# Performance work log

Measured on AMD Instinct MI355X. Metric: run time of the kernel, lower is better.

## Reference

```python
import jax, jax.numpy as jnp
import numpy as np

S, B, H, A = 64, 128, 768, 768


def setup_inputs() -> dict:
    key = jax.random.key(0)
    k1, k2, k3, k4, k5, k6, k7 = jax.random.split(key, 7)
    lim = 1.0 / np.sqrt(H)  # torch Linear default init range
    return {
        "topic_output": jax.random.normal(k1, (1, B, H), dtype=jnp.float32),
        "image_output": jax.random.normal(k2, (S, B, H), dtype=jnp.float32),
        "text_output": jax.random.normal(k3, (S, B, H), dtype=jnp.float32),
        "Wq": jax.random.uniform(k4, (H, A), minval=-lim, maxval=lim, dtype=jnp.float32),
        "bq": jax.random.uniform(k5, (A,), minval=-lim, maxval=lim, dtype=jnp.float32),
        "Wv": jax.random.uniform(k6, (S, H, A), minval=-lim, maxval=lim, dtype=jnp.float32),
        "bv": jax.random.uniform(k7, (S, A), minval=-lim, maxval=lim, dtype=jnp.float32),
    }


def reference(topic_output, image_output, text_output, Wq, bq, Wv, bv):
    # Q = topic_q(topic_output).transpose(0,1) -> [B, 1, A]; we keep it [B, A]
    topic = topic_output[0]                      # [B, H]
    Q = topic @ Wq + bq                          # [B, A]

    # Per step i: atten_input = [topic; image_i; text_i] -> [3, B, H]; V_i = v[i](atten_input)
    # Batched over all steps as grouped GEMMs with the per-step weight stack Wv [S, H, A].
    V_topic = jnp.einsum('bh,sha->sba', topic, Wv)        # [S, B, A]
    V_img = jnp.einsum('sbh,sha->sba', image_output, Wv)  # [S, B, A]
    V_txt = jnp.einsum('sbh,sha->sba', text_output, Wv)   # [S, B, A]
    V = jnp.stack([V_topic, V_img, V_txt], axis=2) + bv[:, None, None, :]  # [S, B, 3, A]

    norm = jnp.asarray(1.0 / np.sqrt(A), dtype=Q.dtype)
    scores = jnp.einsum('ba,sbka->sbk', Q, V) * norm       # [S, B, 3]
    attn = jax.nn.softmax(scores, axis=-1)
    return jnp.einsum('sbk,sbka->sba', attn, V)            # [S, B, A]
```

## Files before the change

kernel.cpp:

```cpp
#include <hip/hip_runtime.h>
#include <hip/hip_bf16.h>
#include <math.h>

#define S_ 64
#define B_ 128
#define H_ 768
#define A_ 768

typedef __bf16 bf16_t;
typedef __attribute__((ext_vector_type(8))) __bf16 bf16x8;
typedef __attribute__((ext_vector_type(4))) __bf16 bf16x4;
typedef __attribute__((ext_vector_type(2))) __bf16 bf16x2;
typedef __attribute__((ext_vector_type(4))) float f32x4;

#define TOPIC_N   98304
#define IMG_N   6291456

__device__ __forceinline__ bf16x8 pack8(float4 a, float4 b) {
    bf16x8 o;
    o[0]=(bf16_t)a.x; o[1]=(bf16_t)a.y; o[2]=(bf16_t)a.z; o[3]=(bf16_t)a.w;
    o[4]=(bf16_t)b.x; o[5]=(bf16_t)b.y; o[6]=(bf16_t)b.z; o[7]=(bf16_t)b.w;
    return o;
}

__device__ __forceinline__ void glds16b(const bf16_t* g, bf16_t* l) {
    __builtin_amdgcn_global_load_lds(
        (const __attribute__((address_space(1))) uint32_t*)g,
        (__attribute__((address_space(3))) uint32_t*)l, 16, 0, 0);
}


__global__ __launch_bounds__(256)
void convert_kernel(const float* __restrict__ topic, const float* __restrict__ image,
                    const float* __restrict__ text, bf16_t* __restrict__ out) {
    const int i = blockIdx.x * 256 + threadIdx.x;
    const int T8 = TOPIC_N / 8, I8 = IMG_N / 8;
    const size_t e = (size_t)i * 8;
    const float* src; size_t off;
    if (i < T8)           { src = topic; off = e; }
    else if (i < T8 + I8) { src = image; off = e - TOPIC_N; }
    else                  { src = text;  off = e - TOPIC_N - IMG_N; }
    const float4* p = reinterpret_cast<const float4*>(src + off);
    float4 a = p[0], b = p[1];
    *reinterpret_cast<bf16x8*>(out + e) = pack8(a, b);
}

__global__ __launch_bounds__(512, 4)
void gemm_fused(const float* __restrict__ Wv, const float* __restrict__ Wq,
                const bf16_t* __restrict__ actB,
                const float* __restrict__ bq, const float* __restrict__ bv,
                bf16_t* __restrict__ Vws, float* __restrict__ Qws)
{
    __shared__ bf16_t Al[2][128 * 64];
    __shared__ bf16_t Bl[2][192 * 64];

    const int b0 = blockIdx.x;
    const int xcd = b0 & 7, ii = b0 >> 3;
    const int bid = (xcd < 4) ? (xcd * 97 + ii) : (388 + (xcd - 4) * 96 + ii);

    const int tid = threadIdx.x;
    const bool isQ = (bid >= 768);
    int s, tm, tn;
    if (isQ) { s = S_; tm = 0; tn = bid - 768; }
    else     { s = bid / 12; const int t = bid % 12; tm = t / 4; tn = t % 4; }

    const bf16_t* Apanel;
    if (isQ || tm == 0) Apanel = actB;
    else if (tm == 1)   Apanel = actB + TOPIC_N + (size_t)s * B_ * H_;
    else                Apanel = actB + TOPIC_N + IMG_N + (size_t)s * B_ * H_;
    const float* Wbase = (isQ ? Wq : (Wv + (size_t)s * H_ * A_)) + tn * 192;

    const int wv = tid >> 6, lane = tid & 63;
    const int wr = wv >> 2, wc = wv & 3;
    const int fr = lane & 15, fg = lane >> 4;

    const int wp  = tid >> 4;
    const int wg  = tid & 15;
    const int wk0 = 2 * wp;

    f32x4 acc[4][3];
    #pragma unroll
    for (int i = 0; i < 4; ++i)
        #pragma unroll
        for (int j = 0; j < 3; ++j)
            acc[i][j] = (f32x4){0.f, 0.f, 0.f, 0.f};

    auto stageA = [&](int t1, int buf) {
        const int k0 = t1 * 64;
        #pragma unroll
        for (int q = 0; q < 2; ++q) {
            const int slot = (q * 8 + wv) * 64 + lane;
            const int row = slot >> 3, c = slot & 7;
            glds16b(Apanel + (size_t)row * H_ + k0 + ((c ^ (row & 7)) * 8),
                    &Al[buf][(q * 8 + wv) * 512]);
        }
    };

    f32x4 wreg[6];
    auto loadW = [&](int t1) {
        const float* base = Wbase + (size_t)(t1 * 64 + wk0) * A_;
        #pragma unroll
        for (int j = 0; j < 3; ++j) {
            wreg[2*j]   = *reinterpret_cast<const f32x4*>(base +        wg * 4 + 64 * j);
            wreg[2*j+1] = *reinterpret_cast<const f32x4*>(base + A_ +   wg * 4 + 64 * j);
        }
    };
    auto writeB = [&](int buf) {
        #pragma unroll
        for (int j = 0; j < 3; ++j)
            #pragma unroll
            for (int i = 0; i < 4; ++i) {
                const int n   = wg * 4 + 64 * j + i;
                const int key = (n ^ (n >> 3)) & 7;
                const int kx  = (((wk0 >> 3) ^ key) << 3) + (wk0 & 7);
                bf16x2 pr;
                pr[0] = (bf16_t)wreg[2*j][i];
                pr[1] = (bf16_t)wreg[2*j+1][i];
                *reinterpret_cast<bf16x2*>(&Bl[buf][n * 64 + kx]) = pr;
            }
    };

    loadW(0);
    stageA(0, 0);
    writeB(0);
    asm volatile("s_waitcnt vmcnt(0) lgkmcnt(0)" ::: "memory");
    __builtin_amdgcn_sched_barrier(0);
    __builtin_amdgcn_s_barrier();
    __builtin_amdgcn_sched_barrier(0);

    #pragma unroll
    for (int t = 0; t < 12; ++t) {
        const int cur = t & 1, nxt = cur ^ 1;
        if (t < 11) {
            loadW(t + 1);
            stageA(t + 1, nxt);
        }
        __builtin_amdgcn_sched_barrier(0);

        #pragma unroll
        for (int kk = 0; kk < 2; ++kk) {
            bf16x8 af[4], bf_[3];
            const int kb = kk * 4 + fg;
            #pragma unroll
            for (int mi = 0; mi < 4; ++mi) {
                const int m = wr * 64 + mi * 16 + fr;
                af[mi] = *reinterpret_cast<const bf16x8*>(
                    &Al[cur][m * 64 + ((kb ^ (m & 7)) << 3)]);
            }
            #pragma unroll
            for (int ni = 0; ni < 3; ++ni) {
                const int n   = wc * 48 + ni * 16 + fr;
                const int key = (n ^ (n >> 3)) & 7;
                bf_[ni] = *reinterpret_cast<const bf16x8*>(
                    &Bl[cur][n * 64 + ((kb ^ key) << 3)]);
            }
            #pragma unroll
            for (int mi = 0; mi < 4; ++mi)
                #pragma unroll
                for (int ni = 0; ni < 3; ++ni)
                    acc[mi][ni] = __builtin_amdgcn_mfma_f32_16x16x32_bf16(
                        af[mi], bf_[ni], acc[mi][ni], 0, 0, 0);
        }
        __builtin_amdgcn_sched_barrier(0);

        if (t < 11) {
            writeB(nxt);
            asm volatile("s_waitcnt vmcnt(0) lgkmcnt(0)" ::: "memory");
            __builtin_amdgcn_sched_barrier(0);
            __builtin_amdgcn_s_barrier();
            __builtin_amdgcn_sched_barrier(0);
        }
    }

    if (isQ) {
        #pragma unroll
        for (int ni = 0; ni < 3; ++ni) {
            const int n = tn * 192 + wc * 48 + ni * 16 + fr;
            const float bias = bq[n];
            #pragma unroll
            for (int mi = 0; mi < 4; ++mi)
                #pragma unroll
                for (int j = 0; j < 4; ++j) {
                    const int m = wr * 64 + mi * 16 + fg * 4 + j;
                    Qws[(size_t)m * A_ + n] = acc[mi][ni][j] + bias;
                }
        }
    } else {
        const float* bvrow = bv + (size_t)s * A_;
        #pragma unroll
        for (int ni = 0; ni < 3; ++ni) {
            const int n = tn * 192 + wc * 48 + ni * 16 + fr;
            const float bias = bvrow[n];
            #pragma unroll
            for (int mi = 0; mi < 4; ++mi)
                #pragma unroll
                for (int j = 0; j < 4; ++j) {
                    const int b = wr * 64 + mi * 16 + fg * 4 + j;
                    Vws[(((size_t)s * B_ + b) * 3 + tm) * A_ + n] = (bf16_t)(acc[mi][ni][j] + bias);
                }
        }
    }
}

__global__ __launch_bounds__(256)
void mm_attn_kernel(const bf16_t* __restrict__ Vws,
                    const float* __restrict__ Qws,
                    float* __restrict__ out)
{
    const int wave = threadIdx.x >> 6;
    const int lane = threadIdx.x & 63;
    const int p = blockIdx.x * 4 + wave;
    const int s = p >> 7;
    const int b = p & 127;
    const float*  qrow  = Qws + (size_t)b * A_;
    const bf16_t* vbase = Vws + ((size_t)s * B_ + b) * 3 * A_;

    float4 qv[3];
    bf16x4 vv[3][3];
    float p0 = 0.f, p1 = 0.f, p2 = 0.f;
    #pragma unroll
    for (int j = 0; j < 3; ++j) {
        const int a = lane * 4 + j * 256;
        qv[j]    = *reinterpret_cast<const float4*>(qrow + a);
        vv[0][j] = *reinterpret_cast<const bf16x4*>(vbase + 0*A_ + a);
        vv[1][j] = *reinterpret_cast<const bf16x4*>(vbase + 1*A_ + a);
        vv[2][j] = *reinterpret_cast<const bf16x4*>(vbase + 2*A_ + a);
        p0 += qv[j].x*(float)vv[0][j][0] + qv[j].y*(float)vv[0][j][1]
            + qv[j].z*(float)vv[0][j][2] + qv[j].w*(float)vv[0][j][3];
        p1 += qv[j].x*(float)vv[1][j][0] + qv[j].y*(float)vv[1][j][1]
            + qv[j].z*(float)vv[1][j][2] + qv[j].w*(float)vv[1][j][3];
        p2 += qv[j].x*(float)vv[2][j][0] + qv[j].y*(float)vv[2][j][1]
            + qv[j].z*(float)vv[2][j][2] + qv[j].w*(float)vv[2][j][3];
    }
    #pragma unroll
    for (int d = 1; d < 64; d <<= 1) {
        p0 += __shfl_xor(p0, d);
        p1 += __shfl_xor(p1, d);
        p2 += __shfl_xor(p2, d);
    }
    const float norm = 0.03608439182435161f;
    const float s0 = p0 * norm, s1 = p1 * norm, s2 = p2 * norm;
    const float mx = fmaxf(s0, fmaxf(s1, s2));
    const float e0 = expf(s0 - mx), e1 = expf(s1 - mx), e2 = expf(s2 - mx);
    const float inv = 1.f / (e0 + e1 + e2);
    const float a0 = e0 * inv, a1 = e1 * inv, a2 = e2 * inv;

    float* orow = out + ((size_t)s * B_ + b) * A_;
    #pragma unroll
    for (int j = 0; j < 3; ++j) {
        const int a = lane * 4 + j * 256;
        float4 o;
        o.x = a0*(float)vv[0][j][0] + a1*(float)vv[1][j][0] + a2*(float)vv[2][j][0];
        o.y = a0*(float)vv[0][j][1] + a1*(float)vv[1][j][1] + a2*(float)vv[2][j][1];
        o.z = a0*(float)vv[0][j][2] + a1*(float)vv[1][j][2] + a2*(float)vv[2][j][2];
        o.w = a0*(float)vv[0][j][3] + a1*(float)vv[1][j][3] + a2*(float)vv[2][j][3];
        *reinterpret_cast<float4*>(orow + a) = o;
    }
}

#define LDSPAD 40
__global__ __launch_bounds__(256, 2)
void mm_gemm_kernel(const float* __restrict__ topic,
                    const float* __restrict__ image,
                    const float* __restrict__ text,
                    const float* __restrict__ Wq,
                    const float* __restrict__ bq,
                    const float* __restrict__ Wv,
                    const float* __restrict__ bv,
                    bf16_t* __restrict__ Vws,
                    float*  __restrict__ Qws)
{
    __shared__ bf16_t Alds[128][LDSPAD];
    __shared__ bf16_t Blds[128][LDSPAD];

    const int bid = blockIdx.x;
    const int tid = threadIdx.x;
    const bool isQ = (bid >= S_ * 18);
    int s, tm, tn;
    if (isQ) { s = 0; tm = 0; tn = bid - S_ * 18; }
    else     { s = bid / 18; const int t = bid % 18; tm = t / 6; tn = t % 6; }

    const int ar  = tid >> 1;
    const int aks = (tid & 1) * 16;
    const float* arow;
    if (isQ) {
        arow = topic + (size_t)ar * H_;
    } else {
        const int am  = tm * 128 + ar;
        const int sel = am >> 7;
        const int b   = am & 127;
        if (sel == 0)      arow = topic + (size_t)b * H_;
        else if (sel == 1) arow = image + ((size_t)s * B_ + b) * H_;
        else               arow = text  + ((size_t)s * B_ + b) * H_;
    }
    const int arot = (ar >> 3) & 3;

    const int bn  = tid & 127;
    const int bks = (tid >> 7) * 16;
    const float* wbase = isQ ? Wq : (Wv + (size_t)s * H_ * A_);
    const float* bcolp = wbase + (size_t)(tn * 128 + bn);
    const int brot = (bn >> 3) & 3;

    const int wave = tid >> 6;
    const int lane = tid & 63;
    const int wr = wave >> 1;
    const int wc = wave & 1;
    const int fr = lane & 15;
    const int fg = lane >> 4;

    f32x4 acc[4][4];
    #pragma unroll
    for (int i = 0; i < 4; ++i)
        #pragma unroll
        for (int j = 0; j < 4; ++j)
            acc[i][j] = (f32x4){0.f, 0.f, 0.f, 0.f};

    for (int k0 = 0; k0 < H_; k0 += 32) {
        float4 av[4];
        const float4* ap = reinterpret_cast<const float4*>(arow + k0 + aks);
        #pragma unroll
        for (int i = 0; i < 4; ++i) av[i] = ap[i];
        float bvr[16];
        #pragma unroll
        for (int j = 0; j < 16; ++j) bvr[j] = bcolp[(size_t)(k0 + bks + j) * A_];

        __syncthreads();

        #pragma unroll
        for (int i = 0; i < 4; ++i) {
            const int j = (i + arot) & 3;
            bf16x4 c;
            c[0] = (bf16_t)av[j].x; c[1] = (bf16_t)av[j].y;
            c[2] = (bf16_t)av[j].z; c[3] = (bf16_t)av[j].w;
            *reinterpret_cast<bf16x4*>(&Alds[ar][aks + 4*j]) = c;
        }
        #pragma unroll
        for (int i = 0; i < 4; ++i) {
            const int j = (i + brot) & 3;
            bf16x4 c;
            c[0] = (bf16_t)bvr[4*j+0]; c[1] = (bf16_t)bvr[4*j+1];
            c[2] = (bf16_t)bvr[4*j+2]; c[3] = (bf16_t)bvr[4*j+3];
            *reinterpret_cast<bf16x4*>(&Blds[bn][bks + 4*j]) = c;
        }
        __syncthreads();

        bf16x8 afrag[4], bfrag[4];
        #pragma unroll
        for (int mi = 0; mi < 4; ++mi)
            afrag[mi] = *reinterpret_cast<const bf16x8*>(&Alds[wr*64 + mi*16 + fr][fg*8]);
        #pragma unroll
        for (int ni = 0; ni < 4; ++ni)
            bfrag[ni] = *reinterpret_cast<const bf16x8*>(&Blds[wc*64 + ni*16 + fr][fg*8]);
        #pragma unroll
        for (int mi = 0; mi < 4; ++mi)
            #pragma unroll
            for (int ni = 0; ni < 4; ++ni)
                acc[mi][ni] = __builtin_amdgcn_mfma_f32_16x16x32_bf16(
                    afrag[mi], bfrag[ni], acc[mi][ni], 0, 0, 0);
    }

    if (isQ) {
        #pragma unroll
        for (int ni = 0; ni < 4; ++ni) {
            const int n = tn*128 + wc*64 + ni*16 + fr;
            const float bias = bq[n];
            #pragma unroll
            for (int mi = 0; mi < 4; ++mi)
                #pragma unroll
                for (int j = 0; j < 4; ++j) {
                    const int m = wr*64 + mi*16 + fg*4 + j;
                    Qws[(size_t)m * A_ + n] = acc[mi][ni][j] + bias;
                }
        }
    } else {
        const float* bvrow = bv + (size_t)s * A_;
        #pragma unroll
        for (int ni = 0; ni < 4; ++ni) {
            const int n = tn*128 + wc*64 + ni*16 + fr;
            const float bias = bvrow[n];
            #pragma unroll
            for (int mi = 0; mi < 4; ++mi)
                #pragma unroll
                for (int j = 0; j < 4; ++j) {
                    const int b = wr*64 + mi*16 + fg*4 + j;
                    Vws[(((size_t)s * B_ + b) * 3 + tm) * A_ + n] = (bf16_t)(acc[mi][ni][j] + bias);
                }
        }
    }
}

extern "C" void kernel_launch(void* const* d_in, const int* in_sizes, int n_in,
                              void* d_out, int out_size, void* d_ws, size_t ws_size,
                              hipStream_t stream)
{
    const float* topic = (const float*)d_in[0];
    const float* image = (const float*)d_in[1];
    const float* text  = (const float*)d_in[2];
    const float* Wq    = (const float*)d_in[3];
    const float* bq    = (const float*)d_in[4];
    const float* Wv    = (const float*)d_in[5];
    const float* bv    = (const float*)d_in[6];
    float* out = (float*)d_out;

    const size_t szAct = (size_t)(TOPIC_N + 2 * IMG_N) * sizeof(bf16_t);
    const size_t szV   = (size_t)S_ * B_ * 3 * A_ * sizeof(bf16_t);
    const size_t szQ   = (size_t)B_ * A_ * sizeof(float);
    const size_t need  = szAct + szV + szQ;

    if (ws_size >= need) {
        char* w = (char*)d_ws;
        bf16_t* actB = (bf16_t*)w;  w += szAct;
        bf16_t* Vws  = (bf16_t*)w;  w += szV;
        float*  Qws  = (float*) w;

        convert_kernel<<<(TOPIC_N + 2 * IMG_N) / 8 / 256, 256, 0, stream>>>(topic, image, text, actB);
        gemm_fused<<<772, 512, 0, stream>>>(Wv, Wq, actB, bq, bv, Vws, Qws);
        mm_attn_kernel<<<S_ * B_ / 4, 256, 0, stream>>>(Vws, Qws, out);
    } else {
        bf16_t* Vws = (bf16_t*)d_ws;
        float*  Qws = (float*)((char*)d_ws + szV);
        mm_gemm_kernel<<<S_ * 18 + 6, 256, 0, stream>>>(topic, image, text, Wq, bq, Wv, bv, Vws, Qws);
        mm_attn_kernel<<<S_ * B_ / 4, 256, 0, stream>>>(Vws, Qws, out);
    }
}
```

Before: 92.92 us.

## Fuse fp32-to-bf16 activation conversion into GEMM with register-staged prefetch

Removes the separate conversion kernel and its bf16 activation workspace. The GEMM now loads fp32 activations straight into registers and converts them to bf16 while writing LDS, in the same way weights were already handled. Global loads are issued two tiles ahead, so the wait before each barrier only covers LDS traffic. This saves a kernel launch and a full write and re-read of the converted activations. In exchange each block reads twice as many bytes of fp32 activation and carries more registers for prefetch, which may limit occupancy.

After: 151.5 us. +63.0%, slower.

```diff
diff --git a/kernel.cpp b/kernel.cpp
--- a/kernel.cpp
+++ b/kernel.cpp
@@ -13,43 +13,20 @@
 typedef __attribute__((ext_vector_type(2))) __bf16 bf16x2;
 typedef __attribute__((ext_vector_type(4))) float f32x4;
 
-#define TOPIC_N   98304
-#define IMG_N   6291456
-
-__device__ __forceinline__ bf16x8 pack8(float4 a, float4 b) {
+__device__ __forceinline__ bf16x8 pack8(f32x4 a, f32x4 b) {
     bf16x8 o;
-    o[0]=(bf16_t)a.x; o[1]=(bf16_t)a.y; o[2]=(bf16_t)a.z; o[3]=(bf16_t)a.w;
-    o[4]=(bf16_t)b.x; o[5]=(bf16_t)b.y; o[6]=(bf16_t)b.z; o[7]=(bf16_t)b.w;
+    o[0]=(bf16_t)a[0]; o[1]=(bf16_t)a[1]; o[2]=(bf16_t)a[2]; o[3]=(bf16_t)a[3];
+    o[4]=(bf16_t)b[0]; o[5]=(bf16_t)b[1]; o[6]=(bf16_t)b[2]; o[7]=(bf16_t)b[3];
     return o;
 }
 
-__device__ __forceinline__ void glds16b(const bf16_t* g, bf16_t* l) {
-    __builtin_amdgcn_global_load_lds(
-        (const __attribute__((address_space(1))) uint32_t*)g,
-        (__attribute__((address_space(3))) uint32_t*)l, 16, 0, 0);
-}
-
-
-__global__ __launch_bounds__(256)
-void convert_kernel(const float* __restrict__ topic, const float* __restrict__ image,
-                    const float* __restrict__ text, bf16_t* __restrict__ out) {
-    const int i = blockIdx.x * 256 + threadIdx.x;
-    const int T8 = TOPIC_N / 8, I8 = IMG_N / 8;
-    const size_t e = (size_t)i * 8;
-    const float* src; size_t off;
-    if (i < T8)           { src = topic; off = e; }
-    else if (i < T8 + I8) { src = image; off = e - TOPIC_N; }
-    else                  { src = text;  off = e - TOPIC_N - IMG_N; }
-    const float4* p = reinterpret_cast<const float4*>(src + off);
-    float4 a = p[0], b = p[1];
-    *reinterpret_cast<bf16x8*>(out + e) = pack8(a, b);
-}
 
 __global__ __launch_bounds__(512, 4)
-void gemm_fused(const float* __restrict__ Wv, const float* __restrict__ Wq,
-                const bf16_t* __restrict__ actB,
-                const float* __restrict__ bq, const float* __restrict__ bv,
-                bf16_t* __restrict__ Vws, float* __restrict__ Qws)
+void gemm_all(const float* __restrict__ topic, const float* __restrict__ image,
+              const float* __restrict__ text,  const float* __restrict__ Wq,
+              const float* __restrict__ Wv,
+              const float* __restrict__ bq, const float* __restrict__ bv,
+              bf16_t* __restrict__ Vws, float* __restrict__ Qws)
 {
     __shared__ bf16_t Al[2][128 * 64];
     __shared__ bf16_t Bl[2][192 * 64];
@@ -64,19 +41,22 @@
     if (isQ) { s = S_; tm = 0; tn = bid - 768; }
     else     { s = bid / 12; const int t = bid % 12; tm = t / 4; tn = t % 4; }
 
-    const bf16_t* Apanel;
-    if (isQ || tm == 0) Apanel = actB;
-    else if (tm == 1)   Apanel = actB + TOPIC_N + (size_t)s * B_ * H_;
-    else                Apanel = actB + TOPIC_N + IMG_N + (size_t)s * B_ * H_;
+    const float* Apanel;
+    if (isQ || tm == 0) Apanel = topic;
+    else if (tm == 1)   Apanel = image + (size_t)s * B_ * H_;
+    else                Apanel = text  + (size_t)s * B_ * H_;
     const float* Wbase = (isQ ? Wq : (Wv + (size_t)s * H_ * A_)) + tn * 192;
 
     const int wv = tid >> 6, lane = tid & 63;
     const int wr = wv >> 2, wc = wv & 3;
     const int fr = lane & 15, fg = lane >> 4;
 
-    const int wp  = tid >> 4;
+    const int ar  = tid >> 2;
+    const int akq = (tid & 3) * 16;
+    const float* Ap = Apanel + (size_t)ar * H_ + akq;
     const int wg  = tid & 15;
-    const int wk0 = 2 * wp;
+    const int wk0 = 2 * (tid >> 4);
+    const float* Wp = Wbase + (size_t)wk0 * A_ + wg * 4;
 
     f32x4 acc[4][3];
     #pragma unroll
@@ -85,24 +65,30 @@
         for (int j = 0; j < 3; ++j)
             acc[i][j] = (f32x4){0.f, 0.f, 0.f, 0.f};
 
-    auto stageA = [&](int t1, int buf) {
-        const int k0 = t1 * 64;
+    f32x4 areg[4];
+    f32x4 wreg[6];
+
+    auto loadA = [&](int t1) {
+        const float* p = Ap + t1 * 64;
+        #pragma unroll
+        for (int i = 0; i < 4; ++i)
+            areg[i] = *reinterpret_cast<const f32x4*>(p + 4 * i);
+    };
+    auto loadW = [&](int t1) {
+        const float* p = Wp + (size_t)(t1 * 64) * A_;
+        #pragma unroll
+        for (int j = 0; j < 3; ++j) {
+            wreg[2*j]   = *reinterpret_cast<const f32x4*>(p +      64 * j);
+            wreg[2*j+1] = *reinterpret_cast<const f32x4*>(p + A_ + 64 * j);
+        }
+    };
+    auto writeA = [&](int buf) {
+        const int c0 = (tid & 3) * 2;
         #pragma unroll
         for (int q = 0; q < 2; ++q) {
-            const int slot = (q * 8 + wv) * 64 + lane;
-            const int row = slot >> 3, c = slot & 7;
-            glds16b(Apanel + (size_t)row * H_ + k0 + ((c ^ (row & 7)) * 8),
-                    &Al[buf][(q * 8 + wv) * 512]);
-        }
-    };
-
-    f32x4 wreg[6];
-    auto loadW = [&](int t1) {
-        const float* base = Wbase + (size_t)(t1 * 64 + wk0) * A_;
-        #pragma unroll
-        for (int j = 0; j < 3; ++j) {
-            wreg[2*j]   = *reinterpret_cast<const f32x4*>(base +        wg * 4 + 64 * j);
-            wreg[2*j+1] = *reinterpret_cast<const f32x4*>(base + A_ +   wg * 4 + 64 * j);
+            const int cs = (c0 + q) ^ (ar & 7);
+            *reinterpret_cast<bf16x8*>(&Al[buf][ar * 64 + cs * 8]) =
+                pack8(areg[2*q], areg[2*q+1]);
         }
     };
     auto writeB = [&](int buf) {
@@ -120,10 +106,10 @@
             }
     };
 
-    loadW(0);
-    stageA(0, 0);
-    writeB(0);
-    asm volatile("s_waitcnt vmcnt(0) lgkmcnt(0)" ::: "memory");
+    loadA(0); loadW(0);
+    writeA(0); writeB(0);
+    loadA(1); loadW(1);
+    asm volatile("s_waitcnt lgkmcnt(0)" ::: "memory");
     __builtin_amdgcn_sched_barrier(0);
     __builtin_amdgcn_s_barrier();
     __builtin_amdgcn_sched_barrier(0);
@@ -131,10 +117,8 @@
     #pragma unroll
     for (int t = 0; t < 12; ++t) {
         const int cur = t & 1, nxt = cur ^ 1;
-        if (t < 11) {
-            loadW(t + 1);
-            stageA(t + 1, nxt);
-        }
+        if (t < 11) { writeA(nxt); writeB(nxt); }
+        if (t < 10) { loadA(t + 2); loadW(t + 2); }
         __builtin_amdgcn_sched_barrier(0);
 
         #pragma unroll
@@ -161,11 +145,9 @@
                     acc[mi][ni] = __builtin_amdgcn_mfma_f32_16x16x32_bf16(
                         af[mi], bf_[ni], acc[mi][ni], 0, 0, 0);
         }
-        __builtin_amdgcn_sched_barrier(0);
 
         if (t < 11) {
-            writeB(nxt);
-            asm volatile("s_waitcnt vmcnt(0) lgkmcnt(0)" ::: "memory");
+            asm volatile("s_waitcnt lgkmcnt(0)" ::: "memory");
             __builtin_amdgcn_sched_barrier(0);
             __builtin_amdgcn_s_barrier();
             __builtin_amdgcn_sched_barrier(0);
@@ -402,19 +384,14 @@
     const float* bv    = (const float*)d_in[6];
     float* out = (float*)d_out;
 
-    const size_t szAct = (size_t)(TOPIC_N + 2 * IMG_N) * sizeof(bf16_t);
-    const size_t szV   = (size_t)S_ * B_ * 3 * A_ * sizeof(bf16_t);
-    const size_t szQ   = (size_t)B_ * A_ * sizeof(float);
-    const size_t need  = szAct + szV + szQ;
+    const size_t szV = (size_t)S_ * B_ * 3 * A_ * sizeof(bf16_t);
+    const size_t szQ = (size_t)B_ * A_ * sizeof(float);
+    const size_t need = szV + szQ;
 
     if (ws_size >= need) {
-        char* w = (char*)d_ws;
-        bf16_t* actB = (bf16_t*)w;  w += szAct;
-        bf16_t* Vws  = (bf16_t*)w;  w += szV;
-        float*  Qws  = (float*) w;
-
-        convert_kernel<<<(TOPIC_N + 2 * IMG_N) / 8 / 256, 256, 0, stream>>>(topic, image, text, actB);
-        gemm_fused<<<772, 512, 0, stream>>>(Wv, Wq, actB, bq, bv, Vws, Qws);
+        bf16_t* Vws = (bf16_t*)d_ws;
+        float*  Qws = (float*)((char*)d_ws + szV);
+        gemm_all<<<772, 512, 0, stream>>>(topic, image, text, Wq, Wv, bq, bv, Vws, Qws);
         mm_attn_kernel<<<S_ * B_ / 4, 256, 0, stream>>>(Vws, Qws, out);
     } else {
         bf16_t* Vws = (bf16_t*)d_ws;
```

## Merge the three activation row tiles into one 384-row GEMM block sharing each Wv tile

Applied to the files above, without the earlier changes.

The V/Q GEMM now uses one 384x192 block tile per step. It covers the topic, image and text rows, so each fp32 Wv tile is loaded and converted to bf16 once rather than three times, and the grid drops from 772 to 260 blocks. Each wave now holds a 6x6 MFMA accumulator tile. The weight prefetch runs two k-steps ahead, with partial vmcnt waits, and the bf16 write to LDS happens before the compute. The cost is much larger LDS and register use, one block per CU, and 260 blocks on roughly 256 CUs, which can leave a small tail. The Q blocks also compute 256 wasted rows, whose results are masked on store.

Measured after the change: 132.2 us. +42.2%, slower.

```diff
diff --git a/kernel.cpp b/kernel.cpp
--- a/kernel.cpp
+++ b/kernel.cpp
@@ -16,7 +16,7 @@
 #define TOPIC_N   98304
 #define IMG_N   6291456
 
-__device__ __forceinline__ bf16x8 pack8(float4 a, float4 b) {
+__device__ __forceinline__ bf16x8 pack8f(float4 a, float4 b) {
     bf16x8 o;
     o[0]=(bf16_t)a.x; o[1]=(bf16_t)a.y; o[2]=(bf16_t)a.z; o[3]=(bf16_t)a.w;
     o[4]=(bf16_t)b.x; o[5]=(bf16_t)b.y; o[6]=(bf16_t)b.z; o[7]=(bf16_t)b.w;
@@ -41,68 +41,53 @@
     else if (i < T8 + I8) { src = image; off = e - TOPIC_N; }
     else                  { src = text;  off = e - TOPIC_N - IMG_N; }
     const float4* p = reinterpret_cast<const float4*>(src + off);
-    float4 a = p[0], b = p[1];
-    *reinterpret_cast<bf16x8*>(out + e) = pack8(a, b);
-}
-
-__global__ __launch_bounds__(512, 4)
-void gemm_fused(const float* __restrict__ Wv, const float* __restrict__ Wq,
-                const bf16_t* __restrict__ actB,
-                const float* __restrict__ bq, const float* __restrict__ bv,
-                bf16_t* __restrict__ Vws, float* __restrict__ Qws)
+    *reinterpret_cast<bf16x8*>(out + e) = pack8f(p[0], p[1]);
+}
+
+__global__ __launch_bounds__(512, 1)
+void gemm_384(const float* __restrict__ Wv, const float* __restrict__ Wq,
+              const bf16_t* __restrict__ actB,
+              const float* __restrict__ bq, const float* __restrict__ bv,
+              bf16_t* __restrict__ Vws, float* __restrict__ Qws)
 {
-    __shared__ bf16_t Al[2][128 * 64];
+    __shared__ bf16_t Al[2][384 * 64];
     __shared__ bf16_t Bl[2][192 * 64];
 
     const int b0 = blockIdx.x;
     const int xcd = b0 & 7, ii = b0 >> 3;
-    const int bid = (xcd < 4) ? (xcd * 97 + ii) : (388 + (xcd - 4) * 96 + ii);
+    const int bid = (xcd < 4) ? (xcd * 33 + ii) : (132 + (xcd - 4) * 32 + ii);
 
     const int tid = threadIdx.x;
-    const bool isQ = (bid >= 768);
-    int s, tm, tn;
-    if (isQ) { s = S_; tm = 0; tn = bid - 768; }
-    else     { s = bid / 12; const int t = bid % 12; tm = t / 4; tn = t % 4; }
-
-    const bf16_t* Apanel;
-    if (isQ || tm == 0) Apanel = actB;
-    else if (tm == 1)   Apanel = actB + TOPIC_N + (size_t)s * B_ * H_;
-    else                Apanel = actB + TOPIC_N + IMG_N + (size_t)s * B_ * H_;
+    const bool isQ = (bid >= 256);
+    int s, tn;
+    if (isQ) { s = S_; tn = bid - 256; }
+    else     { s = bid >> 2; tn = bid & 3; }
+
     const float* Wbase = (isQ ? Wq : (Wv + (size_t)s * H_ * A_)) + tn * 192;
 
     const int wv = tid >> 6, lane = tid & 63;
-    const int wr = wv >> 2, wc = wv & 3;
+    const int wr = wv >> 1, wc = wv & 1;
     const int fr = lane & 15, fg = lane >> 4;
 
-    const int wp  = tid >> 4;
     const int wg  = tid & 15;
-    const int wk0 = 2 * wp;
-
-    f32x4 acc[4][3];
-    #pragma unroll
-    for (int i = 0; i < 4; ++i)
-        #pragma unroll
-        for (int j = 0; j < 3; ++j)
+    const int wk0 = 2 * (tid >> 4);
+    const float* Wp = Wbase + (size_t)wk0 * A_ + wg * 4;
+
+    f32x4 acc[6][6];
+    #pragma unroll
+    for (int i = 0; i < 6; ++i)
+        #pragma unroll
+        for (int j = 0; j < 6; ++j)
             acc[i][j] = (f32x4){0.f, 0.f, 0.f, 0.f};
 
-    auto stageA = [&](int t1, int buf) {
-        const int k0 = t1 * 64;
-        #pragma unroll
-        for (int q = 0; q < 2; ++q) {
-            const int slot = (q * 8 + wv) * 64 + lane;
-            const int row = slot >> 3, c = slot & 7;
-            glds16b(Apanel + (size_t)row * H_ + k0 + ((c ^ (row & 7)) * 8),
-                    &Al[buf][(q * 8 + wv) * 512]);
-        }
-    };
-
     f32x4 wreg[6];
+
     auto loadW = [&](int t1) {
-        const float* base = Wbase + (size_t)(t1 * 64 + wk0) * A_;
+        const float* p = Wp + (size_t)(t1 * 64) * A_;
         #pragma unroll
         for (int j = 0; j < 3; ++j) {
-            wreg[2*j]   = *reinterpret_cast<const f32x4*>(base +        wg * 4 + 64 * j);
-            wreg[2*j+1] = *reinterpret_cast<const f32x4*>(base + A_ +   wg * 4 + 64 * j);
+            wreg[2*j]   = *reinterpret_cast<const f32x4*>(p +      64 * j);
+            wreg[2*j+1] = *reinterpret_cast<const f32x4*>(p + A_ + 64 * j);
         }
     };
     auto writeB = [&](int buf) {
@@ -120,10 +105,34 @@
             }
     };
 
+    auto gldsA1 = [&](int q, int k0, int buf) {
+        const int sl  = (q * 8 + wv) * 64 + lane;
+        const int row = sl >> 3, c = sl & 7;
+        const bf16_t* src;
+        if (isQ) {
+            src = actB + (size_t)row * H_;
+        } else {
+            const int sel = row >> 7, b = row & 127;
+            if (sel == 0)      src = actB + (size_t)row * H_;
+            else if (sel == 1) src = actB + TOPIC_N + ((size_t)s * B_ + b) * H_;
+            else               src = actB + TOPIC_N + IMG_N + ((size_t)s * B_ + b) * H_;
+        }
+        glds16b(src + k0 + ((c ^ (row & 7)) * 8), &Al[buf][(q * 8 + wv) * 512]);
+    };
+    auto stageA = [&](int t1, int buf) {
+        const int k0 = t1 * 64;
+        if (isQ) { gldsA1(0, k0, buf); gldsA1(1, k0, buf); }
+        else {
+            #pragma unroll
+            for (int q = 0; q < 6; ++q) gldsA1(q, k0, buf);
+        }
+    };
+
     loadW(0);
     stageA(0, 0);
     writeB(0);
-    asm volatile("s_waitcnt vmcnt(0) lgkmcnt(0)" ::: "memory");
+    loadW(1);
+    asm volatile("s_waitcnt vmcnt(6) lgkmcnt(0)" ::: "memory");
     __builtin_amdgcn_sched_barrier(0);
     __builtin_amdgcn_s_barrier();
     __builtin_amdgcn_sched_barrier(0);
@@ -131,41 +140,38 @@
     #pragma unroll
     for (int t = 0; t < 12; ++t) {
         const int cur = t & 1, nxt = cur ^ 1;
-        if (t < 11) {
-            loadW(t + 1);
-            stageA(t + 1, nxt);
-        }
+        if (t < 11) { writeB(nxt); stageA(t + 1, nxt); }
+        if (t < 10) loadW(t + 2);
         __builtin_amdgcn_sched_barrier(0);
 
         #pragma unroll
         for (int kk = 0; kk < 2; ++kk) {
-            bf16x8 af[4], bf_[3];
+            bf16x8 af[6], bf_[6];
             const int kb = kk * 4 + fg;
             #pragma unroll
-            for (int mi = 0; mi < 4; ++mi) {
-                const int m = wr * 64 + mi * 16 + fr;
+            for (int mi = 0; mi < 6; ++mi) {
+                const int m = wr * 96 + mi * 16 + fr;
                 af[mi] = *reinterpret_cast<const bf16x8*>(
                     &Al[cur][m * 64 + ((kb ^ (m & 7)) << 3)]);
             }
             #pragma unroll
-            for (int ni = 0; ni < 3; ++ni) {
-                const int n   = wc * 48 + ni * 16 + fr;
+            for (int ni = 0; ni < 6; ++ni) {
+                const int n   = wc * 96 + ni * 16 + fr;
                 const int key = (n ^ (n >> 3)) & 7;
                 bf_[ni] = *reinterpret_cast<const bf16x8*>(
                     &Bl[cur][n * 64 + ((kb ^ key) << 3)]);
             }
             #pragma unroll
-            for (int mi = 0; mi < 4; ++mi)
+            for (int mi = 0; mi < 6; ++mi)
                 #pragma unroll
-                for (int ni = 0; ni < 3; ++ni)
+                for (int ni = 0; ni < 6; ++ni)
                     acc[mi][ni] = __builtin_amdgcn_mfma_f32_16x16x32_bf16(
                         af[mi], bf_[ni], acc[mi][ni], 0, 0, 0);
         }
-        __builtin_amdgcn_sched_barrier(0);
 
         if (t < 11) {
-            writeB(nxt);
-            asm volatile("s_waitcnt vmcnt(0) lgkmcnt(0)" ::: "memory");
+            if (t < 10) asm volatile("s_waitcnt vmcnt(6) lgkmcnt(0)" ::: "memory");
+            else        asm volatile("s_waitcnt vmcnt(0) lgkmcnt(0)" ::: "memory");
             __builtin_amdgcn_sched_barrier(0);
             __builtin_amdgcn_s_barrier();
             __builtin_amdgcn_sched_barrier(0);
@@ -174,28 +180,29 @@
 
     if (isQ) {
         #pragma unroll
-        for (int ni = 0; ni < 3; ++ni) {
-            const int n = tn * 192 + wc * 48 + ni * 16 + fr;
+        for (int ni = 0; ni < 6; ++ni) {
+            const int n = tn * 192 + wc * 96 + ni * 16 + fr;
             const float bias = bq[n];
             #pragma unroll
-            for (int mi = 0; mi < 4; ++mi)
+            for (int mi = 0; mi < 6; ++mi)
                 #pragma unroll
                 for (int j = 0; j < 4; ++j) {
-                    const int m = wr * 64 + mi * 16 + fg * 4 + j;
-                    Qws[(size_t)m * A_ + n] = acc[mi][ni][j] + bias;
+                    const int m = wr * 96 + mi * 16 + fg * 4 + j;
+                    if (m < 128) Qws[(size_t)m * A_ + n] = acc[mi][ni][j] + bias;
                 }
         }
     } else {
         const float* bvrow = bv + (size_t)s * A_;
         #pragma unroll
-        for (int ni = 0; ni < 3; ++ni) {
-            const int n = tn * 192 + wc * 48 + ni * 16 + fr;
+        for (int ni = 0; ni < 6; ++ni) {
+            const int n = tn * 192 + wc * 96 + ni * 16 + fr;
             const float bias = bvrow[n];
             #pragma unroll
-            for (int mi = 0; mi < 4; ++mi)
+            for (int mi = 0; mi < 6; ++mi)
                 #pragma unroll
                 for (int j = 0; j < 4; ++j) {
-                    const int b = wr * 64 + mi * 16 + fg * 4 + j;
+                    const int m  = wr * 96 + mi * 16 + fg * 4 + j;
+                    const int tm = m >> 7, b = m & 127;
                     Vws[(((size_t)s * B_ + b) * 3 + tm) * A_ + n] = (bf16_t)(acc[mi][ni][j] + bias);
                 }
         }
@@ -414,7 +421,7 @@
         float*  Qws  = (float*) w;
 
         convert_kernel<<<(TOPIC_N + 2 * IMG_N) / 8 / 256, 256, 0, stream>>>(topic, image, text, actB);
-        gemm_fused<<<772, 512, 0, stream>>>(Wv, Wq, actB, bq, bv, Vws, Qws);
+        gemm_384<<<260, 512, 0, stream>>>(Wv, Wq, actB, bq, bv, Vws, Qws);
         mm_attn_kernel<<<S_ * B_ / 4, 256, 0, stream>>>(Vws, Qws, out);
     } else {
         bf16_t* Vws = (bf16_t*)d_ws;
```
